# Performance work log

Hardware: AMD Instinct MI355X
Metric: run time of the kernel (lower is better)

The kernel has to match this reference:

```python
import jax, jax.numpy as jnp
import numpy as np

N = 50000      # nodes
E = 800000     # edges (avg degree 16)
D_IN = 18      # 3 fields x 6 timesteps
H = 128        # hidden_dim
HEADS = 4
DH = H // HEADS
D_OUT = 3
NEG = 0.2      # LeakyReLU slope
BN_EPS = 1e-5


def leaky(x):
    return jnp.where(x >= 0, x, NEG * x)


def segment_softmax(e, row, n):
    # numerically stable softmax over edges grouped by target node (axis 0)
    m = jax.ops.segment_max(e, row, num_segments=n)
    ex = jnp.exp(e - m[row])
    s = jax.ops.segment_sum(ex, row, num_segments=n)
    return ex / (s[row] + 1e-16)


def single_head_attn(x, row, col, Wv, b, a_src, a_dst):
    h = x @ Wv + b                                   # [N,H] values
    s_src = x @ a_src                                # [N] query scalar (dim=1)
    s_dst = x @ a_dst                                # [N] key scalar
    e = leaky(s_src[row] + s_dst[col])               # [E]
    alpha = segment_softmax(e, row, N)               # [E]
    return jax.ops.segment_sum(alpha[:, None] * h[col], row, num_segments=N)


def multi_head_attn(x, row, col, Wv, b, a_src, a_dst):
    h = jnp.einsum('nd,hde->nhe', x, Wv) + b         # [N,4,32] per-head values
    s_src = x @ a_src.T                              # [N,4] per-head Q (dim=1)
    s_dst = x @ a_dst.T                              # [N,4] per-head K (dim=1)
    e = leaky(s_src[row] + s_dst[col])               # [E,4]
    alpha = segment_softmax(e, row, N)               # [E,4]
    out = jax.ops.segment_sum(alpha[:, :, None] * h[col], row, num_segments=N)
    return out.reshape(N, HEADS * DH)                # concat heads -> [N,128]


def batch_norm_eval(x, g, bt, m, v):
    return (x - m) * jax.lax.rsqrt(v + BN_EPS) * g + bt


def setup_inputs() -> dict:
    key = jax.random.key(0)
    ks = jax.random.split(key, 16)
    rn = lambda k, shp, s=0.05: jax.random.normal(k, shp, dtype=jnp.float32) * s
    return {
        'x': rn(ks[0], (N, D_IN), 1.0),
        'edge_index': jax.random.randint(ks[1], (2, E), 0, N, dtype=jnp.int32),
        'W_in': rn(ks[2], (D_IN, H)),
        'b_in': jnp.zeros((H,), jnp.float32),
        'W_agg': rn(ks[3], (D_IN, H)),
        'b_agg': jnp.zeros((H,), jnp.float32),
        'sh_Wv': rn(ks[4], (2, H, H)),
        'sh_b': jnp.zeros((2, H), jnp.float32),
        'sh_asrc': rn(ks[5], (2, H)),
        'sh_adst': rn(ks[6], (2, H)),
        'mh_Wv': rn(ks[7], (HEADS, H, DH)),
        'mh_b': jnp.zeros((HEADS, DH), jnp.float32),
        'mh_asrc': rn(ks[8], (HEADS, H)),
        'mh_adst': rn(ks[9], (HEADS, H)),
        'bn_gamma': jnp.ones((3, H), jnp.float32),
        'bn_beta': jnp.zeros((3, H), jnp.float32),
        'bn_mean': jnp.zeros((3, H), jnp.float32),
        'bn_var': jnp.ones((3, H), jnp.float32),
        'W_o1': rn(ks[10], (H, H)),
        'b_o1': jnp.zeros((H,), jnp.float32),
        'W_o2': rn(ks[11], (H, D_OUT), 0.01),
        'b_o2': jnp.zeros((D_OUT,), jnp.float32),
    }


def reference(x, edge_index, W_in, b_in, W_agg, b_agg, sh_Wv, sh_b, sh_asrc, sh_adst,
              mh_Wv, mh_b, mh_asrc, mh_adst, bn_gamma, bn_beta, bn_mean, bn_var,
              W_o1, b_o1, W_o2, b_o2):
    row, col = edge_index[0], edge_index[1]

    # explicit neighbor mean aggregation (fused gather-scatter)
    nsum = jax.ops.segment_sum(x[col], row, num_segments=N)     # [N,D_IN]
    deg = jax.ops.segment_sum(jnp.ones((E,), x.dtype), row, num_segments=N)
    nmean = nsum / (deg[:, None] + 1e-8)

    h = (x @ W_in + b_in) + (nmean @ W_agg + b_agg)             # [N,H]
    x0 = h

    # layer 0: single-head attention + BN + residual(x0) + leaky
    h1 = single_head_attn(h, row, col, sh_Wv[0], sh_b[0], sh_asrc[0], sh_adst[0])
    h1 = batch_norm_eval(h1, bn_gamma[0], bn_beta[0], bn_mean[0], bn_var[0])
    h = leaky(x0 + h1)

    # layer 1: multi-head (4 heads, Q/K dim=1) + BN, no residual (i=1), leaky
    h2 = multi_head_attn(h, row, col, mh_Wv, mh_b, mh_asrc, mh_adst)
    h2 = batch_norm_eval(h2, bn_gamma[1], bn_beta[1], bn_mean[1], bn_var[1])
    h = leaky(h2)

    # layer 2: single-head + BN + residual + leaky
    r = h
    h3 = single_head_attn(h, row, col, sh_Wv[1], sh_b[1], sh_asrc[1], sh_adst[1])
    h3 = batch_norm_eval(h3, bn_gamma[2], bn_beta[2], bn_mean[2], bn_var[2])
    h = leaky(r + h3)

    # output head (dropout is a no-op in eval)
    delta = leaky(h @ W_o1 + b_o1) @ W_o2 + b_o2                # [N,3]

    # residual skip from last timestep of the input sequence
    return x[:, -D_OUT:] + delta
```

## Files before the change

### kernel.cpp

```cpp
#include <hip/hip_runtime.h>
#include <math.h>

#define DIN 18
#define HID 128
#define NEGS 0.2f
#define BN_EPS 1e-5f
#define SCHUNK 2048

typedef unsigned short ushort_t;
typedef __attribute__((ext_vector_type(8))) short bf16x8;
typedef __attribute__((ext_vector_type(4))) float f32x4;

__device__ __forceinline__ float leaky(float x){ return x >= 0.f ? x : NEGS * x; }

__device__ __forceinline__ float wred_sum(float v){
  #pragma unroll
  for (int off = 32; off; off >>= 1) v += __shfl_xor(v, off);
  return v;
}

__device__ __forceinline__ ushort_t f2bf(float f){
  union { float f; unsigned u; } v; v.f = f;
  unsigned r = v.u + 0x7FFFu + ((v.u >> 16) & 1u);
  return (ushort_t)(r >> 16);
}
__device__ __forceinline__ float bf_lo(unsigned p){ return __uint_as_float(p << 16); }
__device__ __forceinline__ float bf_hi(unsigned p){ return __uint_as_float(p & 0xFFFF0000u); }

__device__ __forceinline__ float sel4(float v0, float v1, float v2, float v3, int hd){
  float a = (hd & 1) ? v1 : v0;
  float b = (hd & 1) ? v3 : v2;
  return (hd & 2) ? b : a;
}

__global__ void k_deg_rank(const int* __restrict__ row, int* __restrict__ deg,
                           int* __restrict__ rank, int E){
  int i = blockIdx.x * blockDim.x + threadIdx.x;
  if (i < E) rank[i] = atomicAdd(&deg[row[i]], 1);
}

__global__ void k_scan1(const int* __restrict__ deg, int* __restrict__ bsum, int n){
  __shared__ int wtot[4];
  int tid = threadIdx.x, lane = tid & 63, wid = tid >> 6;
  int base = blockIdx.x * SCHUNK + tid * 8;
  int acc = 0;
  #pragma unroll
  for (int j = 0; j < 8; ++j){
    int i = base + j;
    if (i < n) acc += deg[i];
  }
  #pragma unroll
  for (int off = 32; off; off >>= 1) acc += __shfl_xor(acc, off);
  if (lane == 0) wtot[wid] = acc;
  __syncthreads();
  if (tid == 0) bsum[blockIdx.x] = wtot[0] + wtot[1] + wtot[2] + wtot[3];
}

__global__ void k_scan2(int* __restrict__ bsum, int nb){
  int lane = threadIdx.x;
  int carry = 0;
  for (int base = 0; base < nb; base += 64){
    int i = base + lane;
    int v = (i < nb) ? bsum[i] : 0;
    #pragma unroll
    for (int off = 1; off < 64; off <<= 1){
      int u = __shfl_up(v, off);
      if (lane >= off) v += u;
    }
    if (i < nb) bsum[i] = v + carry;
    carry += __shfl(v, 63);
  }
}

__global__ void k_scan3(const int* __restrict__ deg, const int* __restrict__ bsum,
                        int* __restrict__ rowptr, int n){
  __shared__ int wtot[4];
  int tid = threadIdx.x, lane = tid & 63, wid = tid >> 6;
  int base = blockIdx.x * SCHUNK + tid * 8;
  int l[8];
  int acc = 0;
  #pragma unroll
  for (int j = 0; j < 8; ++j){
    int i = base + j;
    acc += (i < n) ? deg[i] : 0;
    l[j] = acc;
  }
  int v = acc;
  #pragma unroll
  for (int off = 1; off < 64; off <<= 1){
    int u = __shfl_up(v, off);
    if (lane >= off) v += u;
  }
  if (lane == 63) wtot[wid] = v;
  __syncthreads();
  int woff = 0;
  for (int w = 0; w < wid; ++w) woff += wtot[w];
  int boff = (blockIdx.x == 0) ? 0 : bsum[blockIdx.x - 1];
  int tpre = boff + woff + (v - acc);
  #pragma unroll
  for (int j = 0; j < 8; ++j){
    int i = base + j;
    if (i < n) rowptr[i + 1] = tpre + l[j];
  }
  if (blockIdx.x == 0 && tid == 0) rowptr[0] = 0;
}

__global__ void k_scatter(const int* __restrict__ row, const int* __restrict__ col,
                          const int* __restrict__ rowptr, const int* __restrict__ rank,
                          int* __restrict__ cols_s, int E){
  int i = blockIdx.x * blockDim.x + threadIdx.x;
  if (i < E){
    cols_s[rowptr[row[i]] + rank[i]] = col[i];
  }
}

__global__ void k_nmean(const float* __restrict__ x, const int* __restrict__ rowptr,
                        const int* __restrict__ cols, float* __restrict__ nmean, int n){
  __shared__ int s_cv[4][64];
  int wid = threadIdx.x >> 6;
  int node = blockIdx.x * 4 + wid;
  if (node >= n) return;
  int lane = threadIdx.x & 63;
  int s = rowptr[node], e = rowptr[node + 1];
  float acc = 0.f;
  for (int j0 = s; j0 < e; j0 += 64){
    int len = min(64, e - j0);
    int cv = (lane < len) ? cols[j0 + lane] : 0;
    s_cv[wid][lane] = cv;
    int k = 0;
    for (; k + 8 <= len; k += 8){
      float p[8];
      #pragma unroll
      for (int u = 0; u < 8; ++u){
        int c = s_cv[wid][k + u];
        p[u] = (lane < DIN) ? x[c * DIN + lane] : 0.f;
      }
      #pragma unroll
      for (int u = 0; u < 8; ++u) acc += p[u];
    }
    for (; k < len; ++k){
      int c = s_cv[wid][k];
      if (lane < DIN) acc += x[c * DIN + lane];
    }
  }
  if (lane < DIN){
    float d = (float)(e - s);
    nmean[node * DIN + lane] = acc / (d + 1e-8f);
  }
}

__global__ void k_h_in(const float* __restrict__ x, const float* __restrict__ nmean,
                       const float* __restrict__ Win, const float* __restrict__ bin,
                       const float* __restrict__ Wagg, const float* __restrict__ bagg,
                       const float* __restrict__ asrc, const float* __restrict__ adst,
                       float* __restrict__ ssrc, float* __restrict__ sdst,
                       float* __restrict__ out, int n){
  int wid = threadIdx.x >> 6;
  int node = blockIdx.x * 4 + wid;
  if (node >= n) return;
  int lane = threadIdx.x & 63;
  float xv = 0.f;
  if (lane < DIN) xv = x[node * DIN + lane];
  else if (lane < 2 * DIN) xv = nmean[node * DIN + (lane - DIN)];
  float acc0 = bin[lane]      + bagg[lane];
  float acc1 = bin[64 + lane] + bagg[64 + lane];
  #pragma unroll
  for (int d = 0; d < DIN; ++d){
    float xd = __shfl(xv, d);
    float nd = __shfl(xv, DIN + d);
    acc0 += xd * Win[d * HID + lane]       + nd * Wagg[d * HID + lane];
    acc1 += xd * Win[d * HID + 64 + lane]  + nd * Wagg[d * HID + 64 + lane];
  }
  out[node * HID + lane]      = acc0;
  out[node * HID + 64 + lane] = acc1;
  float ps = acc0 * asrc[lane] + acc1 * asrc[64 + lane];
  float pd = acc0 * adst[lane] + acc1 * adst[64 + lane];
  ps = wred_sum(ps);
  pd = wred_sum(pd);
  if (lane == 0){ ssrc[node] = ps; sdst[node] = pd; }
}

__global__ void k_wt_sh(const float* __restrict__ W, ushort_t* __restrict__ Wt){
  int i = blockIdx.x * 256 + threadIdx.x;
  int c = i >> 7, d = i & 127;
  Wt[c * HID + d] = f2bf(W[d * HID + c]);
}
__global__ void k_wt_mh(const float* __restrict__ mhWv, ushort_t* __restrict__ Wt){
  int i = blockIdx.x * 256 + threadIdx.x;
  int c = i >> 7, d = i & 127;
  Wt[c * HID + d] = f2bf(mhWv[((c >> 5) * HID + d) * 32 + (c & 31)]);
}

__global__ void k_gemm_mfma(const float* __restrict__ A, const ushort_t* __restrict__ Bt,
                            const float* __restrict__ bias, ushort_t* __restrict__ dstb,
                            float* __restrict__ dstf, int n, int mode){
  int wv = threadIdx.x >> 6, lane = threadIdx.x & 63;
  int r0 = blockIdx.x * 64 + wv * 16;
  int lr = lane & 15, lk = lane >> 4;
  int arow = r0 + lr; if (arow >= n) arow = n - 1;
  const float* Ap = A + (size_t)arow * HID + lk * 8;
  bf16x8 a[4];
  #pragma unroll
  for (int kb = 0; kb < 4; ++kb){
    float4 lo = *(const float4*)(Ap + kb * 32);
    float4 hi = *(const float4*)(Ap + kb * 32 + 4);
    bf16x8 t;
    t[0] = (short)f2bf(lo.x); t[1] = (short)f2bf(lo.y);
    t[2] = (short)f2bf(lo.z); t[3] = (short)f2bf(lo.w);
    t[4] = (short)f2bf(hi.x); t[5] = (short)f2bf(hi.y);
    t[6] = (short)f2bf(hi.z); t[7] = (short)f2bf(hi.w);
    a[kb] = t;
  }
  f32x4 acc[8];
  #pragma unroll
  for (int t = 0; t < 8; ++t) acc[t] = (f32x4){0.f, 0.f, 0.f, 0.f};
  #pragma unroll
  for (int t = 0; t < 8; ++t){
    const ushort_t* Bp = Bt + (size_t)(t * 16 + lr) * HID + lk * 8;
    #pragma unroll
    for (int kb = 0; kb < 4; ++kb){
      bf16x8 b = *(const bf16x8*)(Bp + kb * 32);
      acc[t] = __builtin_amdgcn_mfma_f32_16x16x32_bf16(a[kb], b, acc[t], 0, 0, 0);
    }
  }
  #pragma unroll
  for (int t = 0; t < 8; ++t){
    int col = t * 16 + lr;
    float bs = bias[col];
    #pragma unroll
    for (int j = 0; j < 4; ++j){
      int rr = r0 + lk * 4 + j;
      if (rr < n){
        float v = acc[t][j] + bs;
        if (mode == 2) dstb[(size_t)rr * HID + col] = f2bf(v);
        else           dstf[(size_t)rr * HID + col] = leaky(v);
      }
    }
  }
}

__global__ void k_agg_sh(const int* __restrict__ rowptr, const int* __restrict__ cols,
                         const float* __restrict__ ssrc, const float* __restrict__ sdst,
                         const ushort_t* __restrict__ hv, const float* __restrict__ resid,
                         const float* __restrict__ bng, const float* __restrict__ bnb,
                         const float* __restrict__ bnm, const float* __restrict__ bnv,
                         const float* __restrict__ masrc, const float* __restrict__ madst,
                         float* __restrict__ ossrc, float* __restrict__ osdst,
                         float* __restrict__ out, int n){
  __shared__ int   s_cv[4][64];
  __shared__ float s_ex[4][64];
  int wid = threadIdx.x >> 6;
  int node = blockIdx.x * 4 + wid;
  if (node >= n) return;
  int lane = threadIdx.x & 63;
  const unsigned* hv32 = (const unsigned*)hv;
  int s = rowptr[node], e = rowptr[node + 1];
  float sq = ssrc[node];
  float ssum = 0.f, a0 = 0.f, a1 = 0.f;
  for (int j0 = s; j0 < e; j0 += 64){
    int len = min(64, e - j0);
    int cv = 0; float ex = 0.f;
    if (lane < len){
      cv = cols[j0 + lane];
      ex = __expf(leaky(sq + sdst[cv]));
    }
    ssum += ex;
    s_cv[wid][lane] = cv;
    s_ex[wid][lane] = ex;
    int k = 0;
    for (; k + 16 <= len; k += 16){
      unsigned p[16]; float l[16];
      #pragma unroll
      for (int u = 0; u < 16; ++u){
        int c = s_cv[wid][k + u];
        l[u] = s_ex[wid][k + u];
        p[u] = hv32[c * 64 + lane];
      }
      #pragma unroll
      for (int u = 0; u < 16; ++u){
        a0 += l[u] * bf_lo(p[u]); a1 += l[u] * bf_hi(p[u]);
      }
    }
    for (; k + 8 <= len; k += 8){
      unsigned p[8]; float l[8];
      #pragma unroll
      for (int u = 0; u < 8; ++u){
        int c = s_cv[wid][k + u];
        l[u] = s_ex[wid][k + u];
        p[u] = hv32[c * 64 + lane];
      }
      #pragma unroll
      for (int u = 0; u < 8; ++u){
        a0 += l[u] * bf_lo(p[u]); a1 += l[u] * bf_hi(p[u]);
      }
    }
    for (; k + 4 <= len; k += 4){
      unsigned p[4]; float l[4];
      #pragma unroll
      for (int u = 0; u < 4; ++u){
        int c = s_cv[wid][k + u];
        l[u] = s_ex[wid][k + u];
        p[u] = hv32[c * 64 + lane];
      }
      #pragma unroll
      for (int u = 0; u < 4; ++u){
        a0 += l[u] * bf_lo(p[u]); a1 += l[u] * bf_hi(p[u]);
      }
    }
    for (; k < len; ++k){
      int c = s_cv[wid][k];
      float l = s_ex[wid][k];
      unsigned p = hv32[c * 64 + lane];
      a0 += l * bf_lo(p); a1 += l * bf_hi(p);
    }
  }
  ssum = wred_sum(ssum);
  float inv = 1.f / (ssum + 1e-16f);
  a0 *= inv; a1 *= inv;
  int d0 = 2 * lane, d1 = 2 * lane + 1;
  float v0 = (a0 - bnm[d0]) * rsqrtf(bnv[d0] + BN_EPS) * bng[d0] + bnb[d0];
  float v1 = (a1 - bnm[d1]) * rsqrtf(bnv[d1] + BN_EPS) * bng[d1] + bnb[d1];
  if (resid){ v0 += resid[node * HID + d0]; v1 += resid[node * HID + d1]; }
  float o0 = leaky(v0), o1 = leaky(v1);
  out[node * HID + d0] = o0;
  out[node * HID + d1] = o1;
  if (ossrc){
    #pragma unroll
    for (int h = 0; h < 4; ++h){
      float ps = o0 * masrc[h * HID + d0] + o1 * masrc[h * HID + d1];
      float pd = o0 * madst[h * HID + d0] + o1 * madst[h * HID + d1];
      ps = wred_sum(ps);
      pd = wred_sum(pd);
      if (lane == 0){ ossrc[node * 4 + h] = ps; osdst[node * 4 + h] = pd; }
    }
  }
}

__global__ void k_agg_mh(const int* __restrict__ rowptr, const int* __restrict__ cols,
                         const float* __restrict__ ssrc, const float* __restrict__ sdst,
                         const ushort_t* __restrict__ hv,
                         const float* __restrict__ bng, const float* __restrict__ bnb,
                         const float* __restrict__ bnm, const float* __restrict__ bnv,
                         const float* __restrict__ sasrc, const float* __restrict__ sadst,
                         float* __restrict__ ossrc, float* __restrict__ osdst,
                         float* __restrict__ out, int n){
  __shared__ int    s_cv[4][64];
  __shared__ float4 s_ex[4][64];
  int wid = threadIdx.x >> 6;
  int node = blockIdx.x * 4 + wid;
  if (node >= n) return;
  int lane = threadIdx.x & 63;
  const unsigned* hv32 = (const unsigned*)hv;
  int s = rowptr[node], e = rowptr[node + 1];
  const float4 sq = *(const float4*)&ssrc[node * 4];
  int hd = lane >> 4;
  float s0 = 0.f, s1 = 0.f, s2 = 0.f, s3 = 0.f;
  float a0 = 0.f, a1 = 0.f;
  const float* exw = &s_ex[wid][0].x;
  for (int j0 = s; j0 < e; j0 += 64){
    int len = min(64, e - j0);
    int cv = 0;
    float e0 = 0.f, e1 = 0.f, e2 = 0.f, e3 = 0.f;
    if (lane < len){
      cv = cols[j0 + lane];
      float4 kd = *(const float4*)&sdst[cv * 4];
      e0 = __expf(leaky(sq.x + kd.x)); e1 = __expf(leaky(sq.y + kd.y));
      e2 = __expf(leaky(sq.z + kd.z)); e3 = __expf(leaky(sq.w + kd.w));
    }
    s0 += e0; s1 += e1; s2 += e2; s3 += e3;
    s_cv[wid][lane] = cv;
    s_ex[wid][lane] = make_float4(e0, e1, e2, e3);
    int k = 0;
    for (; k + 16 <= len; k += 16){
      unsigned p[16]; float l[16];
      #pragma unroll
      for (int u = 0; u < 16; ++u){
        int c = s_cv[wid][k + u];
        l[u] = exw[(k + u) * 4 + hd];
        p[u] = hv32[c * 64 + lane];
      }
      #pragma unroll
      for (int u = 0; u < 16; ++u){
        a0 += l[u] * bf_lo(p[u]); a1 += l[u] * bf_hi(p[u]);
      }
    }
    for (; k + 8 <= len; k += 8){
      unsigned p[8]; float l[8];
      #pragma unroll
      for (int u = 0; u < 8; ++u){
        int c = s_cv[wid][k + u];
        l[u] = exw[(k + u) * 4 + hd];
        p[u] = hv32[c * 64 + lane];
      }
      #pragma unroll
      for (int u = 0; u < 8; ++u){
        a0 += l[u] * bf_lo(p[u]); a1 += l[u] * bf_hi(p[u]);
      }
    }
    for (; k + 4 <= len; k += 4){
      unsigned p[4]; float l[4];
      #pragma unroll
      for (int u = 0; u < 4; ++u){
        int c = s_cv[wid][k + u];
        l[u] = exw[(k + u) * 4 + hd];
        p[u] = hv32[c * 64 + lane];
      }
      #pragma unroll
      for (int u = 0; u < 4; ++u){
        a0 += l[u] * bf_lo(p[u]); a1 += l[u] * bf_hi(p[u]);
      }
    }
    for (; k < len; ++k){
      int c = s_cv[wid][k];
      float l = exw[k * 4 + hd];
      unsigned p = hv32[c * 64 + lane];
      a0 += l * bf_lo(p); a1 += l * bf_hi(p);
    }
  }
  s0 = wred_sum(s0); s1 = wred_sum(s1);
  s2 = wred_sum(s2); s3 = wred_sum(s3);
  float i0 = 1.f / (s0 + 1e-16f), i1 = 1.f / (s1 + 1e-16f);
  float i2 = 1.f / (s2 + 1e-16f), i3 = 1.f / (s3 + 1e-16f);
  float ih = sel4(i0, i1, i2, i3, hd);
  a0 *= ih; a1 *= ih;
  int d0 = 2 * lane, d1 = 2 * lane + 1;
  float v0 = (a0 - bnm[d0]) * rsqrtf(bnv[d0] + BN_EPS) * bng[d0] + bnb[d0];
  float v1 = (a1 - bnm[d1]) * rsqrtf(bnv[d1] + BN_EPS) * bng[d1] + bnb[d1];
  float o0 = leaky(v0), o1 = leaky(v1);
  out[node * HID + d0] = o0;
  out[node * HID + d1] = o1;
  float ps = o0 * sasrc[d0] + o1 * sasrc[d1];
  float pd = o0 * sadst[d0] + o1 * sadst[d1];
  ps = wred_sum(ps);
  pd = wred_sum(pd);
  if (lane == 0){ ossrc[node] = ps; osdst[node] = pd; }
}

__global__ void k_out(const float* __restrict__ o1, const float* __restrict__ Wo2,
                      const float* __restrict__ bo2, const float* __restrict__ x,
                      float* __restrict__ out, int n){
  int node = blockIdx.x * 4 + (threadIdx.x >> 6);
  if (node >= n) return;
  int lane = threadIdx.x & 63;
  float a = o1[node * HID + lane], b = o1[node * HID + 64 + lane];
  float p0 = a * Wo2[lane * 3 + 0] + b * Wo2[(lane + 64) * 3 + 0];
  float p1 = a * Wo2[lane * 3 + 1] + b * Wo2[(lane + 64) * 3 + 1];
  float p2 = a * Wo2[lane * 3 + 2] + b * Wo2[(lane + 64) * 3 + 2];
  p0 = wred_sum(p0); p1 = wred_sum(p1); p2 = wred_sum(p2);
  if (lane == 0){
    out[node * 3 + 0] = x[node * DIN + 15] + p0 + bo2[0];
    out[node * 3 + 1] = x[node * DIN + 16] + p1 + bo2[1];
    out[node * 3 + 2] = x[node * DIN + 17] + p2 + bo2[2];
  }
}

extern "C" void kernel_launch(void* const* d_in, const int* in_sizes, int n_in,
                              void* d_out, int out_size, void* d_ws, size_t ws_size,
                              hipStream_t stream){
  const float* x       = (const float*)d_in[0];
  const int*   ei      = (const int*)  d_in[1];
  const float* W_in    = (const float*)d_in[2];
  const float* b_in    = (const float*)d_in[3];
  const float* W_agg   = (const float*)d_in[4];
  const float* b_agg   = (const float*)d_in[5];
  const float* sh_Wv   = (const float*)d_in[6];
  const float* sh_b    = (const float*)d_in[7];
  const float* sh_asrc = (const float*)d_in[8];
  const float* sh_adst = (const float*)d_in[9];
  const float* mh_Wv   = (const float*)d_in[10];
  const float* mh_b    = (const float*)d_in[11];
  const float* mh_asrc = (const float*)d_in[12];
  const float* mh_adst = (const float*)d_in[13];
  const float* bn_g    = (const float*)d_in[14];
  const float* bn_bt   = (const float*)d_in[15];
  const float* bn_m    = (const float*)d_in[16];
  const float* bn_v    = (const float*)d_in[17];
  const float* W_o1    = (const float*)d_in[18];
  const float* b_o1    = (const float*)d_in[19];
  const float* W_o2    = (const float*)d_in[20];
  const float* b_o2    = (const float*)d_in[21];
  float* out = (float*)d_out;

  const int N = in_sizes[0] / DIN;
  const int E = in_sizes[1] / 2;
  const int* row = ei;
  const int* col = ei + E;

  char* w = (char*)d_ws;
  size_t off = 0;
  auto alloc = [&](size_t bytes) -> void* {
    void* p = w + off;
    off = (off + bytes + 255) & ~(size_t)255;
    return p;
  };
  int*      tmp    = (int*)     alloc((size_t)N * 4);
  int*      rowptr = (int*)     alloc((size_t)(N + 1) * 4);
  int*      cols_s = (int*)     alloc((size_t)E * 4);
  int*      rank   = (int*)     alloc((size_t)E * 4);
  int*      bsum   = (int*)     alloc((size_t)1024 * 4);
  float*    nmean  = (float*)   alloc((size_t)N * DIN * 4);
  float*    ssrcA  = (float*)   alloc((size_t)N * 4);
  float*    sdstA  = (float*)   alloc((size_t)N * 4);
  float*    ssrcB  = (float*)   alloc((size_t)N * 4 * 4);
  float*    sdstB  = (float*)   alloc((size_t)N * 4 * 4);
  ushort_t* wt0    = (ushort_t*)alloc((size_t)HID * HID * 2);
  ushort_t* wt1    = (ushort_t*)alloc((size_t)HID * HID * 2);
  ushort_t* wt2    = (ushort_t*)alloc((size_t)HID * HID * 2);
  ushort_t* wt3    = (ushort_t*)alloc((size_t)HID * HID * 2);
  float*    buf0   = (float*)   alloc((size_t)N * HID * 4);
  float*    buf1   = (float*)   alloc((size_t)N * HID * 4);
  float*    buf2   = (float*)   alloc((size_t)N * HID * 4);
  ushort_t* hvb    = (ushort_t*)alloc((size_t)N * HID * 2);

  const int eb = (E + 255) / 256;
  const int nb4 = (N + 3) / 4;
  const int gb = (N + 63) / 64;
  const int nsb = (N + SCHUNK - 1) / SCHUNK;

  hipMemsetAsync(tmp, 0, (size_t)N * 4, stream);
  k_deg_rank<<<eb, 256, 0, stream>>>(row, tmp, rank, E);
  k_scan1<<<nsb, 256, 0, stream>>>(tmp, bsum, N);
  k_scan2<<<1, 64, 0, stream>>>(bsum, nsb);
  k_scan3<<<nsb, 256, 0, stream>>>(tmp, bsum, rowptr, N);
  k_scatter<<<eb, 256, 0, stream>>>(row, col, rowptr, rank, cols_s, E);

  k_wt_sh<<<64, 256, 0, stream>>>(sh_Wv, wt0);
  k_wt_mh<<<64, 256, 0, stream>>>(mh_Wv, wt1);
  k_wt_sh<<<64, 256, 0, stream>>>(sh_Wv + HID * HID, wt2);
  k_wt_sh<<<64, 256, 0, stream>>>(W_o1, wt3);

  k_nmean<<<nb4, 256, 0, stream>>>(x, rowptr, cols_s, nmean, N);
  k_h_in<<<nb4, 256, 0, stream>>>(x, nmean, W_in, b_in, W_agg, b_agg,
                                  sh_asrc, sh_adst, ssrcA, sdstA, buf0, N);

  k_gemm_mfma<<<gb, 256, 0, stream>>>(buf0, wt0, sh_b, hvb, nullptr, N, 2);
  k_agg_sh<<<nb4, 256, 0, stream>>>(rowptr, cols_s, ssrcA, sdstA, hvb, buf0,
                                    bn_g, bn_bt, bn_m, bn_v,
                                    mh_asrc, mh_adst, ssrcB, sdstB, buf1, N);

  k_gemm_mfma<<<gb, 256, 0, stream>>>(buf1, wt1, mh_b, hvb, nullptr, N, 2);
  k_agg_mh<<<nb4, 256, 0, stream>>>(rowptr, cols_s, ssrcB, sdstB, hvb,
                                    bn_g + HID, bn_bt + HID, bn_m + HID, bn_v + HID,
                                    sh_asrc + HID, sh_adst + HID, ssrcA, sdstA, buf0, N);

  k_gemm_mfma<<<gb, 256, 0, stream>>>(buf0, wt2, sh_b + HID, hvb, nullptr, N, 2);
  k_agg_sh<<<nb4, 256, 0, stream>>>(rowptr, cols_s, ssrcA, sdstA, hvb, buf0,
                                    bn_g + 2 * HID, bn_bt + 2 * HID, bn_m + 2 * HID, bn_v + 2 * HID,
                                    nullptr, nullptr, nullptr, nullptr, buf1, N);

  k_gemm_mfma<<<gb, 256, 0, stream>>>(buf1, wt3, b_o1, nullptr, buf2, N, 1);
  k_out<<<nb4, 256, 0, stream>>>(buf2, W_o2, b_o2, x, out, N);
}
```

Measured before the change: 383.4 us.

## Gather neighbor rows with 16-byte loads across quarter-wave edge groups

```diff
diff --git a/kernel.cpp b/kernel.cpp
--- a/kernel.cpp
+++ b/kernel.cpp
@@ -239,6 +239,12 @@
   }
 }
 
+#define CONSUME8(PV, L)                                  \
+  acc[0] += (L) * bf_lo((PV).x); acc[1] += (L) * bf_hi((PV).x); \
+  acc[2] += (L) * bf_lo((PV).y); acc[3] += (L) * bf_hi((PV).y); \
+  acc[4] += (L) * bf_lo((PV).z); acc[5] += (L) * bf_hi((PV).z); \
+  acc[6] += (L) * bf_lo((PV).w); acc[7] += (L) * bf_hi((PV).w);
+
 __global__ void k_agg_sh(const int* __restrict__ rowptr, const int* __restrict__ cols,
                          const float* __restrict__ ssrc, const float* __restrict__ sdst,
                          const ushort_t* __restrict__ hv, const float* __restrict__ resid,
@@ -253,10 +259,14 @@
   int node = blockIdx.x * 4 + wid;
   if (node >= n) return;
   int lane = threadIdx.x & 63;
-  const unsigned* hv32 = (const unsigned*)hv;
+  int g = lane & 15, q = lane >> 4;
+  const uint4* hvr = (const uint4*)hv;
   int s = rowptr[node], e = rowptr[node + 1];
   float sq = ssrc[node];
-  float ssum = 0.f, a0 = 0.f, a1 = 0.f;
+  float ssum = 0.f;
+  float acc[8];
+  #pragma unroll
+  for (int j = 0; j < 8; ++j) acc[j] = 0.f;
   for (int j0 = s; j0 < e; j0 += 64){
     int len = min(64, e - j0);
     int cv = 0; float ex = 0.f;
@@ -269,68 +279,57 @@
     s_ex[wid][lane] = ex;
     int k = 0;
     for (; k + 16 <= len; k += 16){
-      unsigned p[16]; float l[16];
-      #pragma unroll
-      for (int u = 0; u < 16; ++u){
-        int c = s_cv[wid][k + u];
-        l[u] = s_ex[wid][k + u];
-        p[u] = hv32[c * 64 + lane];
-      }
-      #pragma unroll
-      for (int u = 0; u < 16; ++u){
-        a0 += l[u] * bf_lo(p[u]); a1 += l[u] * bf_hi(p[u]);
-      }
-    }
-    for (; k + 8 <= len; k += 8){
-      unsigned p[8]; float l[8];
-      #pragma unroll
-      for (int u = 0; u < 8; ++u){
-        int c = s_cv[wid][k + u];
-        l[u] = s_ex[wid][k + u];
-        p[u] = hv32[c * 64 + lane];
-      }
-      #pragma unroll
-      for (int u = 0; u < 8; ++u){
-        a0 += l[u] * bf_lo(p[u]); a1 += l[u] * bf_hi(p[u]);
-      }
-    }
-    for (; k + 4 <= len; k += 4){
-      unsigned p[4]; float l[4];
-      #pragma unroll
-      for (int u = 0; u < 4; ++u){
-        int c = s_cv[wid][k + u];
-        l[u] = s_ex[wid][k + u];
-        p[u] = hv32[c * 64 + lane];
-      }
-      #pragma unroll
-      for (int u = 0; u < 4; ++u){
-        a0 += l[u] * bf_lo(p[u]); a1 += l[u] * bf_hi(p[u]);
-      }
-    }
-    for (; k < len; ++k){
-      int c = s_cv[wid][k];
-      float l = s_ex[wid][k];
-      unsigned p = hv32[c * 64 + lane];
-      a0 += l * bf_lo(p); a1 += l * bf_hi(p);
-    }
+      int   c0 = s_cv[wid][k + q],      c1 = s_cv[wid][k + 4 + q];
+      int   c2 = s_cv[wid][k + 8 + q],  c3 = s_cv[wid][k + 12 + q];
+      float l0 = s_ex[wid][k + q],      l1 = s_ex[wid][k + 4 + q];
+      float l2 = s_ex[wid][k + 8 + q],  l3 = s_ex[wid][k + 12 + q];
+      uint4 p0 = hvr[c0 * 16 + g], p1 = hvr[c1 * 16 + g];
+      uint4 p2 = hvr[c2 * 16 + g], p3 = hvr[c3 * 16 + g];
+      CONSUME8(p0, l0); CONSUME8(p1, l1); CONSUME8(p2, l2); CONSUME8(p3, l3);
+    }
+    for (; k < len; k += 4){
+      int kk = k + q;
+      int c = 0; float l = 0.f;
+      if (kk < len){ c = s_cv[wid][kk]; l = s_ex[wid][kk]; }
+      uint4 p = hvr[c * 16 + g];
+      CONSUME8(p, l);
+    }
+  }
+  #pragma unroll
+  for (int j = 0; j < 8; ++j){
+    acc[j] += __shfl_xor(acc[j], 16);
+    acc[j] += __shfl_xor(acc[j], 32);
   }
   ssum = wred_sum(ssum);
   float inv = 1.f / (ssum + 1e-16f);
-  a0 *= inv; a1 *= inv;
-  int d0 = 2 * lane, d1 = 2 * lane + 1;
-  float v0 = (a0 - bnm[d0]) * rsqrtf(bnv[d0] + BN_EPS) * bng[d0] + bnb[d0];
-  float v1 = (a1 - bnm[d1]) * rsqrtf(bnv[d1] + BN_EPS) * bng[d1] + bnb[d1];
-  if (resid){ v0 += resid[node * HID + d0]; v1 += resid[node * HID + d1]; }
-  float o0 = leaky(v0), o1 = leaky(v1);
-  out[node * HID + d0] = o0;
-  out[node * HID + d1] = o1;
+  int dbase = node * HID + 8 * g;
+  float o[8];
+  #pragma unroll
+  for (int j = 0; j < 8; ++j){
+    int d = 8 * g + j;
+    float v = (acc[j] * inv - bnm[d]) * rsqrtf(bnv[d] + BN_EPS) * bng[d] + bnb[d];
+    if (resid) v += resid[dbase + j];
+    o[j] = leaky(v);
+  }
+  if (q == 0){
+    #pragma unroll
+    for (int j = 0; j < 8; ++j) out[dbase + j] = o[j];
+  }
   if (ossrc){
     #pragma unroll
     for (int h = 0; h < 4; ++h){
-      float ps = o0 * masrc[h * HID + d0] + o1 * masrc[h * HID + d1];
-      float pd = o0 * madst[h * HID + d0] + o1 * madst[h * HID + d1];
-      ps = wred_sum(ps);
-      pd = wred_sum(pd);
+      float ps = 0.f, pd = 0.f;
+      #pragma unroll
+      for (int j = 0; j < 8; ++j){
+        int d = 8 * g + j;
+        ps += o[j] * masrc[h * HID + d];
+        pd += o[j] * madst[h * HID + d];
+      }
+      #pragma unroll
+      for (int off = 8; off; off >>= 1){
+        ps += __shfl_xor(ps, off);
+        pd += __shfl_xor(pd, off);
+      }
       if (lane == 0){ ossrc[node * 4 + h] = ps; osdst[node * 4 + h] = pd; }
     }
   }
@@ -350,12 +349,15 @@
   int node = blockIdx.x * 4 + wid;
   if (node >= n) return;
   int lane = threadIdx.x & 63;
-  const unsigned* hv32 = (const unsigned*)hv;
+  int g = lane & 15, q = lane >> 4;
+  int hh = g >> 2;
+  const uint4* hvr = (const uint4*)hv;
   int s = rowptr[node], e = rowptr[node + 1];
   const float4 sq = *(const float4*)&ssrc[node * 4];
-  int hd = lane >> 4;
   float s0 = 0.f, s1 = 0.f, s2 = 0.f, s3 = 0.f;
-  float a0 = 0.f, a1 = 0.f;
+  float acc[8];
+  #pragma unroll
+  for (int j = 0; j < 8; ++j) acc[j] = 0.f;
   const float* exw = &s_ex[wid][0].x;
   for (int j0 = s; j0 < e; j0 += 64){
     int len = min(64, e - j0);
@@ -372,67 +374,56 @@
     s_ex[wid][lane] = make_float4(e0, e1, e2, e3);
     int k = 0;
     for (; k + 16 <= len; k += 16){
-      unsigned p[16]; float l[16];
-      #pragma unroll
-      for (int u = 0; u < 16; ++u){
-        int c = s_cv[wid][k + u];
-        l[u] = exw[(k + u) * 4 + hd];
-        p[u] = hv32[c * 64 + lane];
-      }
-      #pragma unroll
-      for (int u = 0; u < 16; ++u){
-        a0 += l[u] * bf_lo(p[u]); a1 += l[u] * bf_hi(p[u]);
-      }
-    }
-    for (; k + 8 <= len; k += 8){
-      unsigned p[8]; float l[8];
-      #pragma unroll
-      for (int u = 0; u < 8; ++u){
-        int c = s_cv[wid][k + u];
-        l[u] = exw[(k + u) * 4 + hd];
-        p[u] = hv32[c * 64 + lane];
-      }
-      #pragma unroll
-      for (int u = 0; u < 8; ++u){
-        a0 += l[u] * bf_lo(p[u]); a1 += l[u] * bf_hi(p[u]);
-      }
-    }
-    for (; k + 4 <= len; k += 4){
-      unsigned p[4]; float l[4];
-      #pragma unroll
-      for (int u = 0; u < 4; ++u){
-        int c = s_cv[wid][k + u];
-        l[u] = exw[(k + u) * 4 + hd];
-        p[u] = hv32[c * 64 + lane];
-      }
-      #pragma unroll
-      for (int u = 0; u < 4; ++u){
-        a0 += l[u] * bf_lo(p[u]); a1 += l[u] * bf_hi(p[u]);
-      }
-    }
-    for (; k < len; ++k){
-      int c = s_cv[wid][k];
-      float l = exw[k * 4 + hd];
-      unsigned p = hv32[c * 64 + lane];
-      a0 += l * bf_lo(p); a1 += l * bf_hi(p);
-    }
+      int   c0 = s_cv[wid][k + q],      c1 = s_cv[wid][k + 4 + q];
+      int   c2 = s_cv[wid][k + 8 + q],  c3 = s_cv[wid][k + 12 + q];
+      float l0 = exw[(k + q) * 4 + hh],      l1 = exw[(k + 4 + q) * 4 + hh];
+      float l2 = exw[(k + 8 + q) * 4 + hh],  l3 = exw[(k + 12 + q) * 4 + hh];
+      uint4 p0 = hvr[c0 * 16 + g], p1 = hvr[c1 * 16 + g];
+      uint4 p2 = hvr[c2 * 16 + g], p3 = hvr[c3 * 16 + g];
+      CONSUME8(p0, l0); CONSUME8(p1, l1); CONSUME8(p2, l2); CONSUME8(p3, l3);
+    }
+    for (; k < len; k += 4){
+      int kk = k + q;
+      int c = 0; float l = 0.f;
+      if (kk < len){ c = s_cv[wid][kk]; l = exw[kk * 4 + hh]; }
+      uint4 p = hvr[c * 16 + g];
+      CONSUME8(p, l);
+    }
+  }
+  #pragma unroll
+  for (int j = 0; j < 8; ++j){
+    acc[j] += __shfl_xor(acc[j], 16);
+    acc[j] += __shfl_xor(acc[j], 32);
   }
   s0 = wred_sum(s0); s1 = wred_sum(s1);
   s2 = wred_sum(s2); s3 = wred_sum(s3);
   float i0 = 1.f / (s0 + 1e-16f), i1 = 1.f / (s1 + 1e-16f);
   float i2 = 1.f / (s2 + 1e-16f), i3 = 1.f / (s3 + 1e-16f);
-  float ih = sel4(i0, i1, i2, i3, hd);
-  a0 *= ih; a1 *= ih;
-  int d0 = 2 * lane, d1 = 2 * lane + 1;
-  float v0 = (a0 - bnm[d0]) * rsqrtf(bnv[d0] + BN_EPS) * bng[d0] + bnb[d0];
-  float v1 = (a1 - bnm[d1]) * rsqrtf(bnv[d1] + BN_EPS) * bng[d1] + bnb[d1];
-  float o0 = leaky(v0), o1 = leaky(v1);
-  out[node * HID + d0] = o0;
-  out[node * HID + d1] = o1;
-  float ps = o0 * sasrc[d0] + o1 * sasrc[d1];
-  float pd = o0 * sadst[d0] + o1 * sadst[d1];
-  ps = wred_sum(ps);
-  pd = wred_sum(pd);
+  float ih = sel4(i0, i1, i2, i3, hh);
+  int dbase = node * HID + 8 * g;
+  float o[8];
+  #pragma unroll
+  for (int j = 0; j < 8; ++j){
+    int d = 8 * g + j;
+    float v = (acc[j] * ih - bnm[d]) * rsqrtf(bnv[d] + BN_EPS) * bng[d] + bnb[d];
+    o[j] = leaky(v);
+  }
+  if (q == 0){
+    #pragma unroll
+    for (int j = 0; j < 8; ++j) out[dbase + j] = o[j];
+  }
+  float ps = 0.f, pd = 0.f;
+  #pragma unroll
+  for (int j = 0; j < 8; ++j){
+    int d = 8 * g + j;
+    ps += o[j] * sasrc[d];
+    pd += o[j] * sadst[d];
+  }
+  #pragma unroll
+  for (int off = 8; off; off >>= 1){
+    ps += __shfl_xor(ps, off);
+    pd += __shfl_xor(pd, off);
+  }
   if (lane == 0){ ossrc[node] = ps; osdst[node] = pd; }
 }
 
```

After: 783.6 us. +104.4%, slower.

## Store hidden activations in bf16 and fuse output MLP into final GEMM

Applied to the files above, without the earlier changes.

```diff
diff --git a/kernel.cpp b/kernel.cpp
--- a/kernel.cpp
+++ b/kernel.cpp
@@ -26,6 +26,9 @@
 }
 __device__ __forceinline__ float bf_lo(unsigned p){ return __uint_as_float(p << 16); }
 __device__ __forceinline__ float bf_hi(unsigned p){ return __uint_as_float(p & 0xFFFF0000u); }
+__device__ __forceinline__ unsigned packbf(float a, float b){
+  return (unsigned)f2bf(a) | ((unsigned)f2bf(b) << 16);
+}
 
 __device__ __forceinline__ float sel4(float v0, float v1, float v2, float v3, int hd){
   float a = (hd & 1) ? v1 : v0;
@@ -154,7 +157,7 @@
                        const float* __restrict__ Wagg, const float* __restrict__ bagg,
                        const float* __restrict__ asrc, const float* __restrict__ adst,
                        float* __restrict__ ssrc, float* __restrict__ sdst,
-                       float* __restrict__ out, int n){
+                       ushort_t* __restrict__ out, int n){
   int wid = threadIdx.x >> 6;
   int node = blockIdx.x * 4 + wid;
   if (node >= n) return;
@@ -171,8 +174,8 @@
     acc0 += xd * Win[d * HID + lane]       + nd * Wagg[d * HID + lane];
     acc1 += xd * Win[d * HID + 64 + lane]  + nd * Wagg[d * HID + 64 + lane];
   }
-  out[node * HID + lane]      = acc0;
-  out[node * HID + 64 + lane] = acc1;
+  out[node * HID + lane]      = f2bf(acc0);
+  out[node * HID + 64 + lane] = f2bf(acc1);
   float ps = acc0 * asrc[lane] + acc1 * asrc[64 + lane];
   float pd = acc0 * adst[lane] + acc1 * adst[64 + lane];
   ps = wred_sum(ps);
@@ -191,26 +194,17 @@
   Wt[c * HID + d] = f2bf(mhWv[((c >> 5) * HID + d) * 32 + (c & 31)]);
 }
 
-__global__ void k_gemm_mfma(const float* __restrict__ A, const ushort_t* __restrict__ Bt,
+__global__ void k_gemm_mfma(const ushort_t* __restrict__ A, const ushort_t* __restrict__ Bt,
                             const float* __restrict__ bias, ushort_t* __restrict__ dstb,
-                            float* __restrict__ dstf, int n, int mode){
+                            int n){
   int wv = threadIdx.x >> 6, lane = threadIdx.x & 63;
   int r0 = blockIdx.x * 64 + wv * 16;
   int lr = lane & 15, lk = lane >> 4;
   int arow = r0 + lr; if (arow >= n) arow = n - 1;
-  const float* Ap = A + (size_t)arow * HID + lk * 8;
+  const ushort_t* Ap = A + (size_t)arow * HID + lk * 8;
   bf16x8 a[4];
   #pragma unroll
-  for (int kb = 0; kb < 4; ++kb){
-    float4 lo = *(const float4*)(Ap + kb * 32);
-    float4 hi = *(const float4*)(Ap + kb * 32 + 4);
-    bf16x8 t;
-    t[0] = (short)f2bf(lo.x); t[1] = (short)f2bf(lo.y);
-    t[2] = (short)f2bf(lo.z); t[3] = (short)f2bf(lo.w);
-    t[4] = (short)f2bf(hi.x); t[5] = (short)f2bf(hi.y);
-    t[6] = (short)f2bf(hi.z); t[7] = (short)f2bf(hi.w);
-    a[kb] = t;
-  }
+  for (int kb = 0; kb < 4; ++kb) a[kb] = *(const bf16x8*)(Ap + kb * 32);
   f32x4 acc[8];
   #pragma unroll
   for (int t = 0; t < 8; ++t) acc[t] = (f32x4){0.f, 0.f, 0.f, 0.f};
@@ -230,23 +224,69 @@
     #pragma unroll
     for (int j = 0; j < 4; ++j){
       int rr = r0 + lk * 4 + j;
-      if (rr < n){
-        float v = acc[t][j] + bs;
-        if (mode == 2) dstb[(size_t)rr * HID + col] = f2bf(v);
-        else           dstf[(size_t)rr * HID + col] = leaky(v);
-      }
+      if (rr < n) dstb[(size_t)rr * HID + col] = f2bf(acc[t][j] + bs);
+    }
+  }
+}
+
+__global__ void k_gemm_out(const ushort_t* __restrict__ A, const ushort_t* __restrict__ Bt,
+                           const float* __restrict__ bias, const float* __restrict__ Wo2,
+                           const float* __restrict__ bo2, const float* __restrict__ x,
+                           float* __restrict__ out, int n){
+  int wv = threadIdx.x >> 6, lane = threadIdx.x & 63;
+  int r0 = blockIdx.x * 64 + wv * 16;
+  int lr = lane & 15, lk = lane >> 4;
+  int arow = r0 + lr; if (arow >= n) arow = n - 1;
+  const ushort_t* Ap = A + (size_t)arow * HID + lk * 8;
+  bf16x8 a[4];
+  #pragma unroll
+  for (int kb = 0; kb < 4; ++kb) a[kb] = *(const bf16x8*)(Ap + kb * 32);
+  f32x4 acc[8];
+  #pragma unroll
+  for (int t = 0; t < 8; ++t) acc[t] = (f32x4){0.f, 0.f, 0.f, 0.f};
+  #pragma unroll
+  for (int t = 0; t < 8; ++t){
+    const ushort_t* Bp = Bt + (size_t)(t * 16 + lr) * HID + lk * 8;
+    #pragma unroll
+    for (int kb = 0; kb < 4; ++kb){
+      bf16x8 b = *(const bf16x8*)(Bp + kb * 32);
+      acc[t] = __builtin_amdgcn_mfma_f32_16x16x32_bf16(a[kb], b, acc[t], 0, 0, 0);
+    }
+  }
+  #pragma unroll
+  for (int j = 0; j < 4; ++j){
+    float p0 = 0.f, p1 = 0.f, p2 = 0.f;
+    #pragma unroll
+    for (int t = 0; t < 8; ++t){
+      int col = t * 16 + lr;
+      float v = leaky(acc[t][j] + bias[col]);
+      p0 += v * Wo2[col * 3 + 0];
+      p1 += v * Wo2[col * 3 + 1];
+      p2 += v * Wo2[col * 3 + 2];
+    }
+    #pragma unroll
+    for (int off = 1; off < 16; off <<= 1){
+      p0 += __shfl_xor(p0, off);
+      p1 += __shfl_xor(p1, off);
+      p2 += __shfl_xor(p2, off);
+    }
+    int rr = r0 + lk * 4 + j;
+    if (lr == 0 && rr < n){
+      out[rr * 3 + 0] = x[rr * DIN + 15] + p0 + bo2[0];
+      out[rr * 3 + 1] = x[rr * DIN + 16] + p1 + bo2[1];
+      out[rr * 3 + 2] = x[rr * DIN + 17] + p2 + bo2[2];
     }
   }
 }
 
 __global__ void k_agg_sh(const int* __restrict__ rowptr, const int* __restrict__ cols,
                          const float* __restrict__ ssrc, const float* __restrict__ sdst,
-                         const ushort_t* __restrict__ hv, const float* __restrict__ resid,
+                         const ushort_t* __restrict__ hv, const ushort_t* __restrict__ resid,
                          const float* __restrict__ bng, const float* __restrict__ bnb,
                          const float* __restrict__ bnm, const float* __restrict__ bnv,
                          const float* __restrict__ masrc, const float* __restrict__ madst,
                          float* __restrict__ ossrc, float* __restrict__ osdst,
-                         float* __restrict__ out, int n){
+                         ushort_t* __restrict__ out, int n){
   __shared__ int   s_cv[4][64];
   __shared__ float s_ex[4][64];
   int wid = threadIdx.x >> 6;
@@ -320,10 +360,12 @@
   int d0 = 2 * lane, d1 = 2 * lane + 1;
   float v0 = (a0 - bnm[d0]) * rsqrtf(bnv[d0] + BN_EPS) * bng[d0] + bnb[d0];
   float v1 = (a1 - bnm[d1]) * rsqrtf(bnv[d1] + BN_EPS) * bng[d1] + bnb[d1];
-  if (resid){ v0 += resid[node * HID + d0]; v1 += resid[node * HID + d1]; }
+  if (resid){
+    unsigned rv = *(const unsigned*)&resid[node * HID + d0];
+    v0 += bf_lo(rv); v1 += bf_hi(rv);
+  }
   float o0 = leaky(v0), o1 = leaky(v1);
-  out[node * HID + d0] = o0;
-  out[node * HID + d1] = o1;
+  *(unsigned*)&out[node * HID + d0] = packbf(o0, o1);
   if (ossrc){
     #pragma unroll
     for (int h = 0; h < 4; ++h){
@@ -343,7 +385,7 @@
                          const float* __restrict__ bnm, const float* __restrict__ bnv,
                          const float* __restrict__ sasrc, const float* __restrict__ sadst,
                          float* __restrict__ ossrc, float* __restrict__ osdst,
-                         float* __restrict__ out, int n){
+                         ushort_t* __restrict__ out, int n){
   __shared__ int    s_cv[4][64];
   __shared__ float4 s_ex[4][64];
   int wid = threadIdx.x >> 6;
@@ -427,31 +469,12 @@
   float v0 = (a0 - bnm[d0]) * rsqrtf(bnv[d0] + BN_EPS) * bng[d0] + bnb[d0];
   float v1 = (a1 - bnm[d1]) * rsqrtf(bnv[d1] + BN_EPS) * bng[d1] + bnb[d1];
   float o0 = leaky(v0), o1 = leaky(v1);
-  out[node * HID + d0] = o0;
-  out[node * HID + d1] = o1;
+  *(unsigned*)&out[node * HID + d0] = packbf(o0, o1);
   float ps = o0 * sasrc[d0] + o1 * sasrc[d1];
   float pd = o0 * sadst[d0] + o1 * sadst[d1];
   ps = wred_sum(ps);
   pd = wred_sum(pd);
   if (lane == 0){ ossrc[node] = ps; osdst[node] = pd; }
-}
-
-__global__ void k_out(const float* __restrict__ o1, const float* __restrict__ Wo2,
-                      const float* __restrict__ bo2, const float* __restrict__ x,
-                      float* __restrict__ out, int n){
-  int node = blockIdx.x * 4 + (threadIdx.x >> 6);
-  if (node >= n) return;
-  int lane = threadIdx.x & 63;
-  float a = o1[node * HID + lane], b = o1[node * HID + 64 + lane];
-  float p0 = a * Wo2[lane * 3 + 0] + b * Wo2[(lane + 64) * 3 + 0];
-  float p1 = a * Wo2[lane * 3 + 1] + b * Wo2[(lane + 64) * 3 + 1];
-  float p2 = a * Wo2[lane * 3 + 2] + b * Wo2[(lane + 64) * 3 + 2];
-  p0 = wred_sum(p0); p1 = wred_sum(p1); p2 = wred_sum(p2);
-  if (lane == 0){
-    out[node * 3 + 0] = x[node * DIN + 15] + p0 + bo2[0];
-    out[node * 3 + 1] = x[node * DIN + 16] + p1 + bo2[1];
-    out[node * 3 + 2] = x[node * DIN + 17] + p2 + bo2[2];
-  }
 }
 
 extern "C" void kernel_launch(void* const* d_in, const int* in_sizes, int n_in,
@@ -507,9 +530,8 @@
   ushort_t* wt1    = (ushort_t*)alloc((size_t)HID * HID * 2);
   ushort_t* wt2    = (ushort_t*)alloc((size_t)HID * HID * 2);
   ushort_t* wt3    = (ushort_t*)alloc((size_t)HID * HID * 2);
-  float*    buf0   = (float*)   alloc((size_t)N * HID * 4);
-  float*    buf1   = (float*)   alloc((size_t)N * HID * 4);
-  float*    buf2   = (float*)   alloc((size_t)N * HID * 4);
+  ushort_t* b0     = (ushort_t*)alloc((size_t)N * HID * 2);
+  ushort_t* b1     = (ushort_t*)alloc((size_t)N * HID * 2);
   ushort_t* hvb    = (ushort_t*)alloc((size_t)N * HID * 2);
 
   const int eb = (E + 255) / 256;
@@ -531,23 +553,22 @@
 
   k_nmean<<<nb4, 256, 0, stream>>>(x, rowptr, cols_s, nmean, N);
   k_h_in<<<nb4, 256, 0, stream>>>(x, nmean, W_in, b_in, W_agg, b_agg,
-                                  sh_asrc, sh_adst, ssrcA, sdstA, buf0, N);
-
-  k_gemm_mfma<<<gb, 256, 0, stream>>>(buf0, wt0, sh_b, hvb, nullptr, N, 2);
-  k_agg_sh<<<nb4, 256, 0, stream>>>(rowptr, cols_s, ssrcA, sdstA, hvb, buf0,
+                                  sh_asrc, sh_adst, ssrcA, sdstA, b0, N);
+
+  k_gemm_mfma<<<gb, 256, 0, stream>>>(b0, wt0, sh_b, hvb, N);
+  k_agg_sh<<<nb4, 256, 0, stream>>>(rowptr, cols_s, ssrcA, sdstA, hvb, b0,
                                     bn_g, bn_bt, bn_m, bn_v,
-                                    mh_asrc, mh_adst, ssrcB, sdstB, buf1, N);
-
-  k_gemm_mfma<<<gb, 256, 0, stream>>>(buf1, wt1, mh_b, hvb, nullptr, N, 2);
+                                    mh_asrc, mh_adst, ssrcB, sdstB, b1, N);
+
+  k_gemm_mfma<<<gb, 256, 0, stream>>>(b1, wt1, mh_b, hvb, N);
   k_agg_mh<<<nb4, 256, 0, stream>>>(rowptr, cols_s, ssrcB, sdstB, hvb,
                                     bn_g + HID, bn_bt + HID, bn_m + HID, bn_v + HID,
-                                    sh_asrc + HID, sh_adst + HID, ssrcA, sdstA, buf0, N);
-
-  k_gemm_mfma<<<gb, 256, 0, stream>>>(buf0, wt2, sh_b + HID, hvb, nullptr, N, 2);
-  k_agg_sh<<<nb4, 256, 0, stream>>>(rowptr, cols_s, ssrcA, sdstA, hvb, buf0,
+                                    sh_asrc + HID, sh_adst + HID, ssrcA, sdstA, b0, N);
+
+  k_gemm_mfma<<<gb, 256, 0, stream>>>(b0, wt2, sh_b + HID, hvb, N);
+  k_agg_sh<<<nb4, 256, 0, stream>>>(rowptr, cols_s, ssrcA, sdstA, hvb, b0,
                                     bn_g + 2 * HID, bn_bt + 2 * HID, bn_m + 2 * HID, bn_v + 2 * HID,
-                                    nullptr, nullptr, nullptr, nullptr, buf1, N);
-
-  k_gemm_mfma<<<gb, 256, 0, stream>>>(buf1, wt3, b_o1, nullptr, buf2, N, 1);
-  k_out<<<nb4, 256, 0, stream>>>(buf2, W_o2, b_o2, x, out, N);
-}
+                                    nullptr, nullptr, nullptr, nullptr, b1, N);
+
+  k_gemm_out<<<gb, 256, 0, stream>>>(b1, wt3, b_o1, W_o2, b_o2, x, out, N);
+}
```

New measurement: 369.2 us. 3.7% less time.
